# Kernel tuning notes

Hardware: AMD Instinct MI355X
Metric: run time of the kernel (lower is better)

The kernel has to match this reference:

```python
import jax, jax.numpy as jnp
import numpy as np

N_NODES = 100000
N_HYPEREDGES = 10000
NNZ = 1600000

def setup_inputs() -> dict:
    key = jax.random.key(0)
    k = jax.random.split(key, 7)
    return {
        "x": jax.random.normal(k[0], (N_NODES, 1), dtype=jnp.float32),
        "W1": jax.random.normal(k[1], (1, 128), dtype=jnp.float32) * 0.5,
        "b1": jax.random.normal(k[2], (128,), dtype=jnp.float32) * 0.1,
        "W2": jax.random.normal(k[3], (128, 1), dtype=jnp.float32) * 0.1,
        "b2": jax.random.normal(k[4], (1,), dtype=jnp.float32) * 0.1,
        "node_idx": jax.random.randint(k[5], (NNZ,), 0, N_NODES, dtype=jnp.int64),
        "edge_idx": jax.random.randint(k[6], (NNZ,), 0, N_HYPEREDGES, dtype=jnp.int64),
    }

def _hypergraph_conv(x, W, b, node_idx, edge_idx, n_nodes, n_edges):
    # PyG HypergraphConv (use_attention=False, hyperedge_weight=1):
    # out = D^-1 H B^-1 H^T (X W) + b
    x = x @ W  # [N, F_out]
    ones = jnp.ones(node_idx.shape[0], dtype=x.dtype)
    D = jax.ops.segment_sum(ones, node_idx, num_segments=n_nodes)   # node degree
    B = jax.ops.segment_sum(ones, edge_idx, num_segments=n_edges)   # hyperedge degree
    D_inv = jnp.where(D > 0, 1.0 / D, 0.0)
    B_inv = jnp.where(B > 0, 1.0 / B, 0.0)
    # node -> hyperedge: e = B^-1 H^T x
    e = B_inv[:, None] * jax.ops.segment_sum(x[node_idx], edge_idx, num_segments=n_edges)
    # hyperedge -> node: out = D^-1 H e
    out = D_inv[:, None] * jax.ops.segment_sum(e[edge_idx], node_idx, num_segments=n_nodes)
    return out + b

def reference(x, W1, b1, W2, b2, node_idx, edge_idx):
    n_nodes = x.shape[0]
    h = _hypergraph_conv(x, W1, b1, node_idx, edge_idx, n_nodes, N_HYPEREDGES)
    h = jax.nn.relu(h)
    out = _hypergraph_conv(h, W2, b2, node_idx, edge_idx, n_nodes, N_HYPEREDGES)
    return out
```

## Files before the change

kernel.cpp:

```cpp
#include <hip/hip_runtime.h>

static constexpr int N_NODES = 100000;
static constexpr int N_EDGES = 10000;
static constexpr int NNZ     = 1600000;

static constexpr int G1    = 256;
static constexpr int CHUNK = NNZ / G1;
static constexpr int NRN   = 250;
static constexpr int RN    = 400;
static constexpr int NRE   = 250;
static constexpr int RE    = 40;
static constexpr int SLOT  = 64;
static constexpr int BLK   = 1024;
static constexpr int NW    = 16;
static constexpr int GF    = 250;


__device__ __forceinline__ float ld_a(const float* p) {
    return __hip_atomic_load(p, __ATOMIC_RELAXED, __HIP_MEMORY_SCOPE_AGENT);
}
__device__ __forceinline__ void st_a(float* p, float v) {
    __hip_atomic_store(p, v, __ATOMIC_RELAXED, __HIP_MEMORY_SCOPE_AGENT);
}

__device__ __forceinline__ void bar_arrive(unsigned* bar, int phase) {
    __syncthreads();
    if (threadIdx.x == 0)
        __hip_atomic_fetch_add(bar + phase * 256 + (blockIdx.x & 7) * 32, 1u,
                               __ATOMIC_RELAXED, __HIP_MEMORY_SCOPE_AGENT);
}
__device__ __forceinline__ void bar_wait(unsigned* bar, int phase) {
    if (threadIdx.x == 0) {
        unsigned* flag = bar + 768 + phase * 32;
        if (blockIdx.x == 0) {
            unsigned* cnt = bar + phase * 256;
            unsigned sum;
            do {
                __builtin_amdgcn_s_sleep(2);
                sum = 0u;
                #pragma unroll
                for (int g = 0; g < 8; ++g)
                    sum += __hip_atomic_load(cnt + g * 32, __ATOMIC_RELAXED,
                                             __HIP_MEMORY_SCOPE_AGENT);
            } while (sum < (unsigned)GF);
            __hip_atomic_store(flag, 1u, __ATOMIC_RELAXED, __HIP_MEMORY_SCOPE_AGENT);
        } else {
            while (__hip_atomic_load(flag, __ATOMIC_RELAXED,
                                     __HIP_MEMORY_SCOPE_AGENT) == 0u)
                __builtin_amdgcn_s_sleep(2);
        }
    }
    __syncthreads();
}

__global__ __launch_bounds__(BLK) void k_bin(
        const int* __restrict__ nidx, const int* __restrict__ eidx,
        unsigned* __restrict__ binN, unsigned* __restrict__ binE,
        unsigned* __restrict__ cntN, unsigned* __restrict__ cntE,
        unsigned* __restrict__ bar) {
    __shared__ unsigned cN[NRN], cE[NRE];
    if (blockIdx.x == 0 && threadIdx.x < 896) bar[threadIdx.x] = 0u;
    for (int j = threadIdx.x; j < NRN; j += BLK) cN[j] = 0u;
    for (int j = threadIdx.x; j < NRE; j += BLK) cE[j] = 0u;
    __syncthreads();
    const int b = blockIdx.x;
    const int i0 = b * CHUNK, i1 = i0 + CHUNK;
    for (int i = i0 + threadIdx.x; i < i1; i += BLK) {
        int n = nidx[i], e = eidx[i];
        int rn = n / RN;
        int re = e / RE;
        unsigned pn = atomicAdd(&cN[rn], 1u);
        unsigned pe = atomicAdd(&cE[re], 1u);
        binN[((size_t)rn * G1 + b) * SLOT + pn] = ((unsigned)(n - rn * RN) << 14) | (unsigned)e;
        binE[((size_t)re * G1 + b) * SLOT + pe] = ((unsigned)(e - re * RE) << 17) | (unsigned)n;
    }
    __syncthreads();
    for (int j = threadIdx.x; j < NRN; j += BLK) cntN[(size_t)j * G1 + b] = cN[j];
    for (int j = threadIdx.x; j < NRE; j += BLK) cntE[(size_t)j * G1 + b] = cE[j];
}

__global__ __launch_bounds__(BLK) void k_fused(
        const unsigned* __restrict__ binN, const unsigned* __restrict__ binE,
        const unsigned* __restrict__ cntN, const unsigned* __restrict__ cntE,
        const float* __restrict__ x,
        const float* __restrict__ W1, const float* __restrict__ b1,
        const float* __restrict__ W2, const float* __restrict__ b2,
        float* __restrict__ v1, float* __restrict__ v2, float* __restrict__ P_S,
        unsigned* __restrict__ bar, float* __restrict__ out) {
    __shared__ float    sBig[N_EDGES];
    __shared__ float    eS[NW][RE];
    __shared__ unsigned eC[NW][RE];
    __shared__ float    sS_n[RN];
    __shared__ unsigned sC_n[RN];
    __shared__ unsigned scntE[G1];
    __shared__ unsigned scntN[G1];
    __shared__ float    wgt[384];
    __shared__ float    y_loc[RN];

    const int b = blockIdx.x;
    const int t = threadIdx.x;
    const int wv = t >> 6;
    float my_binv = 0.0f;
    float my_dinv = 0.0f;

    for (int j = t; j < NW * RE; j += BLK) { (&eS[0][0])[j] = 0.0f; (&eC[0][0])[j] = 0u; }
    if (t < G1) scntE[t] = cntE[(size_t)b * G1 + t];
    __syncthreads();
    {
        const unsigned* baseE = binE + (size_t)b * G1 * SLOT;
        for (int j = t; j < G1 * SLOT; j += BLK) {
            int s = j & (SLOT - 1), bb = j >> 6;
            if ((unsigned)s < scntE[bb]) {
                unsigned w = baseE[j];
                atomicAdd(&eS[wv][w >> 17], x[w & 0x1FFFFu]);
                atomicAdd(&eC[wv][w >> 17], 1u);
            }
        }
        __syncthreads();
        if (t < RE) {
            float s = 0.0f; unsigned c = 0u;
            #pragma unroll
            for (int k = 0; k < NW; ++k) { s += eS[k][t]; c += eC[k][t]; }
            my_binv = (c > 0u) ? (1.0f / (float)c) : 0.0f;
            st_a(&v1[b * RE + t], s * my_binv);
        }
    }
    bar_arrive(bar, 0);
    if (t < RN) { sS_n[t] = 0.0f; sC_n[t] = 0u; }
    if (t < G1) scntN[t] = cntN[(size_t)b * G1 + t];
    if (t < 128) { wgt[t] = W1[t]; wgt[128 + t] = b1[t]; wgt[256 + t] = W2[t]; }
    bar_wait(bar, 0);

    const unsigned* baseN = binN + (size_t)b * G1 * SLOT;
    for (int j = t; j < N_EDGES; j += BLK) sBig[j] = ld_a(&v1[j]);
    __syncthreads();
    for (int j = t; j < G1 * SLOT; j += BLK) {
        int s = j & (SLOT - 1), bb = j >> 6;
        if ((unsigned)s < scntN[bb]) {
            unsigned w = baseN[j];
            atomicAdd(&sS_n[w >> 14], sBig[w & 0x3FFFu]);
            atomicAdd(&sC_n[w >> 14], 1u);
        }
    }
    __syncthreads();
    if (t < RN) {
        unsigned c = sC_n[t];
        my_dinv = (c > 0u) ? (1.0f / (float)c) : 0.0f;
        float tt = sS_n[t] * my_dinv;
        float acc = 0.0f;
        #pragma unroll
        for (int f = 0; f < 128; ++f) {
            float h = fmaf(tt, wgt[f], wgt[128 + f]);
            h = fmaxf(h, 0.0f);
            acc = fmaf(h, wgt[256 + f], acc);
        }
        y_loc[t] = acc;
    }
    __syncthreads();
    for (int j = t; j < N_EDGES; j += BLK) sBig[j] = 0.0f;
    __syncthreads();
    for (int j = t; j < G1 * SLOT; j += BLK) {
        int s = j & (SLOT - 1), bb = j >> 6;
        if ((unsigned)s < scntN[bb]) {
            unsigned w = baseN[j];
            atomicAdd(&sBig[w & 0x3FFFu], y_loc[w >> 14]);
        }
    }
    __syncthreads();
    {
        float* ps = P_S + (size_t)b * N_EDGES;
        for (int j = t; j < N_EDGES; j += BLK) st_a(&ps[j], sBig[j]);
    }
    bar_arrive(bar, 1);
    bar_wait(bar, 1);

    {
        const int lane = t & 63;
        if (lane < RE) {
            float acc = 0.0f;
            for (int g = wv; g < GF; g += NW)
                acc += ld_a(&P_S[(size_t)g * N_EDGES + b * RE + lane]);
            eS[wv][lane] = acc;
        }
    }
    __syncthreads();
    if (t < RE) {
        float s = 0.0f;
        #pragma unroll
        for (int k = 0; k < NW; ++k) s += eS[k][t];
        st_a(&v2[b * RE + t], s * my_binv);
    }
    bar_arrive(bar, 2);
    if (t < RN) sS_n[t] = 0.0f;
    bar_wait(bar, 2);

    for (int j = t; j < N_EDGES; j += BLK) sBig[j] = ld_a(&v2[j]);
    __syncthreads();
    for (int j = t; j < G1 * SLOT; j += BLK) {
        int s = j & (SLOT - 1), bb = j >> 6;
        if ((unsigned)s < scntN[bb]) {
            unsigned w = baseN[j];
            atomicAdd(&sS_n[w >> 14], sBig[w & 0x3FFFu]);
        }
    }
    __syncthreads();
    if (t < RN) out[b * RN + t] = fmaf(sS_n[t], my_dinv, b2[0]);
}

extern "C" void kernel_launch(void* const* d_in, const int* in_sizes, int n_in,
                              void* d_out, int out_size, void* d_ws, size_t ws_size,
                              hipStream_t stream) {
    const float* x    = (const float*)d_in[0];
    const float* W1   = (const float*)d_in[1];
    const float* b1   = (const float*)d_in[2];
    const float* W2   = (const float*)d_in[3];
    const float* b2   = (const float*)d_in[4];
    const int*   nidx = (const int*)d_in[5];
    const int*   eidx = (const int*)d_in[6];
    float*       out  = (float*)d_out;

    char* ws = (char*)d_ws;
    unsigned* binN = (unsigned*)(ws + 0);
    unsigned* binE = (unsigned*)(ws + 16384000);
    unsigned* cntN = (unsigned*)(ws + 32768000);
    unsigned* cntE = (unsigned*)(ws + 33024000);
    float*    v1   = (float*)(ws + 33280000);
    float*    v2   = (float*)(ws + 33320000);
    float*    P_S  = (float*)(ws + 33360000);
    unsigned* bar  = (unsigned*)(ws + 43360000);

    k_bin  <<<G1, BLK, 0, stream>>>(nidx, eidx, binN, binE, cntN, cntE, bar);
    k_fused<<<GF, BLK, 0, stream>>>(binN, binE, cntN, cntE, x, W1, b1, W2, b2,
                                    v1, v2, P_S, bar, out);
}
```

Baseline: 85.01 us.

## Fuse first node-to-edge aggregation into binning and cache bin words in registers

The binning kernel now accumulates per-block partial hyperedge sums and packed 16-bit degree counts in shared memory and writes them out. The fused kernel reduces these partials, so the edge-binned copy and its scatter pass are gone. Bin words are loaded once into registers and reused for the three later node-side passes instead of being re-read from global memory. Atomic loads on v1, v2 and P_S are replaced by plain loads. This relies on cache coherence across the software grid barrier and adds a 10 MB partial-sum write plus reduction.

New measurement: 75.34 us (median of 2 runs). 11.4% less time.

```diff
diff --git a/kernel.cpp b/kernel.cpp
--- a/kernel.cpp
+++ b/kernel.cpp
@@ -8,17 +8,14 @@
 static constexpr int CHUNK = NNZ / G1;
 static constexpr int NRN   = 250;
 static constexpr int RN    = 400;
-static constexpr int NRE   = 250;
 static constexpr int RE    = 40;
 static constexpr int SLOT  = 64;
 static constexpr int BLK   = 1024;
 static constexpr int NW    = 16;
 static constexpr int GF    = 250;
-
-
-__device__ __forceinline__ float ld_a(const float* p) {
-    return __hip_atomic_load(p, __ATOMIC_RELAXED, __HIP_MEMORY_SCOPE_AGENT);
-}
+static constexpr int ITER  = G1 * SLOT / BLK;
+
+
 __device__ __forceinline__ void st_a(float* p, float v) {
     __hip_atomic_store(p, v, __ATOMIC_RELAXED, __HIP_MEMORY_SCOPE_AGENT);
 }
@@ -53,36 +50,41 @@
     __syncthreads();
 }
 
-__global__ __launch_bounds__(BLK) void k_bin(
+__global__ __launch_bounds__(BLK) void k_bin_agg(
         const int* __restrict__ nidx, const int* __restrict__ eidx,
-        unsigned* __restrict__ binN, unsigned* __restrict__ binE,
-        unsigned* __restrict__ cntN, unsigned* __restrict__ cntE,
+        const float* __restrict__ x,
+        unsigned* __restrict__ binN, unsigned* __restrict__ cntN,
+        float* __restrict__ P_S1, unsigned* __restrict__ P_B1,
         unsigned* __restrict__ bar) {
-    __shared__ unsigned cN[NRN], cE[NRE];
+    __shared__ float    sS[N_EDGES];
+    __shared__ unsigned sC[N_EDGES / 2];
+    __shared__ unsigned cN[NRN];
     if (blockIdx.x == 0 && threadIdx.x < 896) bar[threadIdx.x] = 0u;
+    for (int j = threadIdx.x; j < N_EDGES; j += BLK) sS[j] = 0.0f;
+    for (int j = threadIdx.x; j < N_EDGES / 2; j += BLK) sC[j] = 0u;
     for (int j = threadIdx.x; j < NRN; j += BLK) cN[j] = 0u;
-    for (int j = threadIdx.x; j < NRE; j += BLK) cE[j] = 0u;
     __syncthreads();
     const int b = blockIdx.x;
     const int i0 = b * CHUNK, i1 = i0 + CHUNK;
     for (int i = i0 + threadIdx.x; i < i1; i += BLK) {
         int n = nidx[i], e = eidx[i];
+        atomicAdd(&sS[e], x[n]);
+        atomicAdd(&sC[e >> 1], 1u << ((e & 1) * 16));
         int rn = n / RN;
-        int re = e / RE;
         unsigned pn = atomicAdd(&cN[rn], 1u);
-        unsigned pe = atomicAdd(&cE[re], 1u);
         binN[((size_t)rn * G1 + b) * SLOT + pn] = ((unsigned)(n - rn * RN) << 14) | (unsigned)e;
-        binE[((size_t)re * G1 + b) * SLOT + pe] = ((unsigned)(e - re * RE) << 17) | (unsigned)n;
     }
     __syncthreads();
     for (int j = threadIdx.x; j < NRN; j += BLK) cntN[(size_t)j * G1 + b] = cN[j];
-    for (int j = threadIdx.x; j < NRE; j += BLK) cntE[(size_t)j * G1 + b] = cE[j];
+    float*    ps = P_S1 + (size_t)b * N_EDGES;
+    unsigned* pb = P_B1 + (size_t)b * (N_EDGES / 2);
+    for (int j = threadIdx.x; j < N_EDGES; j += BLK) ps[j] = sS[j];
+    for (int j = threadIdx.x; j < N_EDGES / 2; j += BLK) pb[j] = sC[j];
 }
 
 __global__ __launch_bounds__(BLK) void k_fused(
-        const unsigned* __restrict__ binN, const unsigned* __restrict__ binE,
-        const unsigned* __restrict__ cntN, const unsigned* __restrict__ cntE,
-        const float* __restrict__ x,
+        const unsigned* __restrict__ binN, const unsigned* __restrict__ cntN,
+        const float* __restrict__ P_S1, const unsigned* __restrict__ P_B1,
         const float* __restrict__ W1, const float* __restrict__ b1,
         const float* __restrict__ W2, const float* __restrict__ b2,
         float* __restrict__ v1, float* __restrict__ v2, float* __restrict__ P_S,
@@ -92,7 +94,6 @@
     __shared__ unsigned eC[NW][RE];
     __shared__ float    sS_n[RN];
     __shared__ unsigned sC_n[RN];
-    __shared__ unsigned scntE[G1];
     __shared__ unsigned scntN[G1];
     __shared__ float    wgt[384];
     __shared__ float    y_loc[RN];
@@ -100,30 +101,26 @@
     const int b = blockIdx.x;
     const int t = threadIdx.x;
     const int wv = t >> 6;
+    const int lane = t & 63;
     float my_binv = 0.0f;
     float my_dinv = 0.0f;
 
-    for (int j = t; j < NW * RE; j += BLK) { (&eS[0][0])[j] = 0.0f; (&eC[0][0])[j] = 0u; }
-    if (t < G1) scntE[t] = cntE[(size_t)b * G1 + t];
-    __syncthreads();
-    {
-        const unsigned* baseE = binE + (size_t)b * G1 * SLOT;
-        for (int j = t; j < G1 * SLOT; j += BLK) {
-            int s = j & (SLOT - 1), bb = j >> 6;
-            if ((unsigned)s < scntE[bb]) {
-                unsigned w = baseE[j];
-                atomicAdd(&eS[wv][w >> 17], x[w & 0x1FFFFu]);
-                atomicAdd(&eC[wv][w >> 17], 1u);
-            }
-        }
-        __syncthreads();
-        if (t < RE) {
-            float s = 0.0f; unsigned c = 0u;
-            #pragma unroll
-            for (int k = 0; k < NW; ++k) { s += eS[k][t]; c += eC[k][t]; }
-            my_binv = (c > 0u) ? (1.0f / (float)c) : 0.0f;
-            st_a(&v1[b * RE + t], s * my_binv);
-        }
+    if (lane < RE) {
+        const int e = b * RE + lane;
+        float s = 0.0f; unsigned c = 0u;
+        for (int g = wv; g < G1; g += NW) {
+            s += P_S1[(size_t)g * N_EDGES + e];
+            c += (P_B1[(size_t)g * (N_EDGES / 2) + (e >> 1)] >> ((e & 1) * 16)) & 0xFFFFu;
+        }
+        eS[wv][lane] = s; eC[wv][lane] = c;
+    }
+    __syncthreads();
+    if (t < RE) {
+        float s = 0.0f; unsigned c = 0u;
+        #pragma unroll
+        for (int k = 0; k < NW; ++k) { s += eS[k][t]; c += eC[k][t]; }
+        my_binv = (c > 0u) ? (1.0f / (float)c) : 0.0f;
+        st_a(&v1[b * RE + t], s * my_binv);
     }
     bar_arrive(bar, 0);
     if (t < RN) { sS_n[t] = 0.0f; sC_n[t] = 0u; }
@@ -132,15 +129,20 @@
     bar_wait(bar, 0);
 
     const unsigned* baseN = binN + (size_t)b * G1 * SLOT;
-    for (int j = t; j < N_EDGES; j += BLK) sBig[j] = ld_a(&v1[j]);
-    __syncthreads();
-    for (int j = t; j < G1 * SLOT; j += BLK) {
-        int s = j & (SLOT - 1), bb = j >> 6;
+    for (int j = t; j < N_EDGES; j += BLK) sBig[j] = v1[j];
+    __syncthreads();
+    unsigned w_reg[ITER];
+    #pragma unroll
+    for (int it = 0; it < ITER; ++it) {
+        const int j = t + it * BLK;
+        const int s = j & (SLOT - 1), bb = j >> 6;
+        unsigned w = 0xFFFFFFFFu;
         if ((unsigned)s < scntN[bb]) {
-            unsigned w = baseN[j];
+            w = baseN[j];
             atomicAdd(&sS_n[w >> 14], sBig[w & 0x3FFFu]);
             atomicAdd(&sC_n[w >> 14], 1u);
         }
+        w_reg[it] = w;
     }
     __syncthreads();
     if (t < RN) {
@@ -159,12 +161,10 @@
     __syncthreads();
     for (int j = t; j < N_EDGES; j += BLK) sBig[j] = 0.0f;
     __syncthreads();
-    for (int j = t; j < G1 * SLOT; j += BLK) {
-        int s = j & (SLOT - 1), bb = j >> 6;
-        if ((unsigned)s < scntN[bb]) {
-            unsigned w = baseN[j];
-            atomicAdd(&sBig[w & 0x3FFFu], y_loc[w >> 14]);
-        }
+    #pragma unroll
+    for (int it = 0; it < ITER; ++it) {
+        unsigned w = w_reg[it];
+        if (w != 0xFFFFFFFFu) atomicAdd(&sBig[w & 0x3FFFu], y_loc[w >> 14]);
     }
     __syncthreads();
     {
@@ -174,14 +174,11 @@
     bar_arrive(bar, 1);
     bar_wait(bar, 1);
 
-    {
-        const int lane = t & 63;
-        if (lane < RE) {
-            float acc = 0.0f;
-            for (int g = wv; g < GF; g += NW)
-                acc += ld_a(&P_S[(size_t)g * N_EDGES + b * RE + lane]);
-            eS[wv][lane] = acc;
-        }
+    if (lane < RE) {
+        float acc = 0.0f;
+        for (int g = wv; g < GF; g += NW)
+            acc += P_S[(size_t)g * N_EDGES + b * RE + lane];
+        eS[wv][lane] = acc;
     }
     __syncthreads();
     if (t < RE) {
@@ -194,14 +191,12 @@
     if (t < RN) sS_n[t] = 0.0f;
     bar_wait(bar, 2);
 
-    for (int j = t; j < N_EDGES; j += BLK) sBig[j] = ld_a(&v2[j]);
-    __syncthreads();
-    for (int j = t; j < G1 * SLOT; j += BLK) {
-        int s = j & (SLOT - 1), bb = j >> 6;
-        if ((unsigned)s < scntN[bb]) {
-            unsigned w = baseN[j];
-            atomicAdd(&sS_n[w >> 14], sBig[w & 0x3FFFu]);
-        }
+    for (int j = t; j < N_EDGES; j += BLK) sBig[j] = v2[j];
+    __syncthreads();
+    #pragma unroll
+    for (int it = 0; it < ITER; ++it) {
+        unsigned w = w_reg[it];
+        if (w != 0xFFFFFFFFu) atomicAdd(&sS_n[w >> 14], sBig[w & 0x3FFFu]);
     }
     __syncthreads();
     if (t < RN) out[b * RN + t] = fmaf(sS_n[t], my_dinv, b2[0]);
@@ -221,15 +216,15 @@
 
     char* ws = (char*)d_ws;
     unsigned* binN = (unsigned*)(ws + 0);
-    unsigned* binE = (unsigned*)(ws + 16384000);
-    unsigned* cntN = (unsigned*)(ws + 32768000);
-    unsigned* cntE = (unsigned*)(ws + 33024000);
-    float*    v1   = (float*)(ws + 33280000);
-    float*    v2   = (float*)(ws + 33320000);
-    float*    P_S  = (float*)(ws + 33360000);
-    unsigned* bar  = (unsigned*)(ws + 43360000);
-
-    k_bin  <<<G1, BLK, 0, stream>>>(nidx, eidx, binN, binE, cntN, cntE, bar);
-    k_fused<<<GF, BLK, 0, stream>>>(binN, binE, cntN, cntE, x, W1, b1, W2, b2,
-                                    v1, v2, P_S, bar, out);
-}
+    unsigned* cntN = (unsigned*)(ws + 16384000);
+    float*    P_S1 = (float*)(ws + 16640000);
+    unsigned* P_B1 = (unsigned*)(ws + 26880000);
+    float*    v1   = (float*)(ws + 32000000);
+    float*    v2   = (float*)(ws + 32040000);
+    float*    P_S  = (float*)(ws + 32080000);
+    unsigned* bar  = (unsigned*)(ws + 42080000);
+
+    k_bin_agg<<<G1, BLK, 0, stream>>>(nidx, eidx, x, binN, cntN, P_S1, P_B1, bar);
+    k_fused  <<<GF, BLK, 0, stream>>>(binN, cntN, P_S1, P_B1, W1, b1, W2, b2,
+                                      v1, v2, P_S, bar, out);
+}
```
